# Optimization experiments

Hardware: AMD Instinct MI355X
Metric: run time of the kernel (lower is better)

## Reference

```python
import jax, jax.numpy as jnp
import numpy as np

B, S, D, H = 2, 2048, 2048, 16
NOPE, ROPE, V, C = 128, 64, 128, 512
EPS = 1e-6


def _rope(x, cos, sin):
    # x: [b,s,h,d] with d even; consecutive pairs form complex numbers (torch view_as_complex)
    b, s, h, d = x.shape
    x2 = x.reshape(b, s, h, d // 2, 2)
    xr, xi = x2[..., 0], x2[..., 1]
    c = cos[None, :, None, :]
    sn = sin[None, :, None, :]
    yr = xr * c - xi * sn
    yi = xr * sn + xi * c
    return jnp.stack([yr, yi], axis=-1).reshape(b, s, h, d)


def _rmsnorm(x, w):
    return x * jax.lax.rsqrt(jnp.mean(x * x, axis=-1, keepdims=True) + EPS) * w


def setup_inputs() -> dict:
    key = jax.random.key(0)
    ks = jax.random.split(key, 6)
    x = jax.random.normal(ks[0], (B, S, D), jnp.float32)
    # xavier-ish scaled weights (torch layout: [out, in])
    wq = jax.random.normal(ks[1], (H * (NOPE + ROPE), D), jnp.float32) * (D ** -0.5)
    wkv_a = jax.random.normal(ks[2], (C + ROPE, D), jnp.float32) * (D ** -0.5)
    kv_norm_w = jnp.ones((C,), jnp.float32)
    wkv_b = jax.random.normal(ks[3], (H * (NOPE + V), C), jnp.float32) * (C ** -0.5)
    wo = jax.random.normal(ks[4], (D, H * V), jnp.float32) * ((H * V) ** -0.5)
    # rope freqs (theta=10000), cos/sin of shape [S, ROPE//2]
    inv = 1.0 / (10000.0 ** (np.arange(0, ROPE, 2, dtype=np.float32) / ROPE))
    ang = np.outer(np.arange(S, dtype=np.float32), inv)
    cos = jnp.asarray(np.cos(ang), jnp.float32)
    sin = jnp.asarray(np.sin(ang), jnp.float32)
    # causal additive mask [S, S]
    idx = jnp.arange(S)
    mask = jnp.where(idx[None, :] <= idx[:, None], 0.0, -1e9).astype(jnp.float32)
    return dict(x=x, cos=cos, sin=sin, mask=mask, wq=wq, wkv_a=wkv_a,
                kv_norm_w=kv_norm_w, wkv_b=wkv_b, wo=wo)


def reference(x, cos, sin, mask, wq, wkv_a, kv_norm_w, wkv_b, wo):
    scale = (NOPE + ROPE) ** -0.5
    # Q projection -> [B,S,H,NOPE+ROPE]
    q = (x @ wq.T).reshape(B, S, H, NOPE + ROPE)
    q_nope, q_pe = q[..., :NOPE], q[..., NOPE:]
    q_pe = _rope(q_pe, cos, sin)
    # low-rank KV latent + shared rope key
    kvr = x @ wkv_a.T                      # [B,S,C+ROPE]
    kv, k_pe = kvr[..., :C], kvr[..., C:]
    k_pe = _rope(k_pe[:, :, None, :], cos, sin)[:, :, 0, :]   # [B,S,ROPE]
    # absorb-mode: fold wkv_b's nope part into q
    wb = wkv_b.reshape(H, NOPE + V, C)
    q_abs = jnp.einsum('bshd,hdc->bshc', q_nope, wb[:, :NOPE])
    kvn = _rmsnorm(kv, kv_norm_w)          # latent cache [B,S,C]
    scores = (jnp.einsum('bshc,btc->bsht', q_abs, kvn)
              + jnp.einsum('bshr,btr->bsht', q_pe, k_pe)) * scale
    scores = scores + mask[None, :, None, :]
    p = jax.nn.softmax(scores.astype(jnp.float32), axis=-1).astype(x.dtype)
    o = jnp.einsum('bsht,btc->bshc', p, kvn)
    o = jnp.einsum('bshc,hdc->bshd', o, wb[:, NOPE:])   # un-absorb value proj
    return o.reshape(B, S, H * V) @ wo.T
```

## Files before the change

### kernel.cpp

```cpp
#include <hip/hip_runtime.h>
#include <hip/hip_bf16.h>

#define B_ 2
#define S_ 2048
#define H_ 16

typedef unsigned short ushort_t;
typedef unsigned int uint_t;
typedef __attribute__((ext_vector_type(8))) short bf16x8;
typedef __attribute__((ext_vector_type(4))) float f32x4;

__device__ __forceinline__ ushort_t f2bf(float f) {
    uint_t u = __float_as_uint(f);
    return (ushort_t)((u + 0x7fffu + ((u >> 16) & 1u)) >> 16);
}
__device__ __forceinline__ float bf2f(ushort_t v) {
    return __uint_as_float(((uint_t)v) << 16);
}

__device__ __forceinline__ void gl_lds16(const ushort_t* g, ushort_t* l) {
    __builtin_amdgcn_global_load_lds(
        (const __attribute__((address_space(1))) unsigned int*)(unsigned long long)g,
        (__attribute__((address_space(3))) unsigned int*)(unsigned int)(unsigned long long)l,
        16, 0, 0);
}

__global__ __launch_bounds__(256) void cast_bf16(const float* __restrict__ src,
                                                 ushort_t* __restrict__ dst, int n)
{
    int i = (blockIdx.x * 256 + threadIdx.x) * 4;
    if (i < n) {
        float4 v = *(const float4*)(src + i);
        ushort_t pk[4] = { f2bf(v.x), f2bf(v.y), f2bf(v.z), f2bf(v.w) };
        *(uint2*)(dst + i) = *(const uint2*)pk;
    }
}

__global__ __launch_bounds__(256) void cast2_bf16(const float* __restrict__ src,
                                                  ushort_t* __restrict__ hi,
                                                  ushort_t* __restrict__ lo, int n)
{
    int i = (blockIdx.x * 256 + threadIdx.x) * 4;
    if (i < n) {
        float4 v = *(const float4*)(src + i);
        float vv[4] = { v.x, v.y, v.z, v.w };
        ushort_t ph[4], pl[4];
#pragma unroll
        for (int k = 0; k < 4; k++) {
            ph[k] = f2bf(vv[k]);
            pl[k] = f2bf(vv[k] - bf2f(ph[k]));
        }
        *(uint2*)(hi + i) = *(const uint2*)ph;
        *(uint2*)(lo + i) = *(const uint2*)pl;
    }
}

__global__ __launch_bounds__(256, 2) void gemm_bf16(const ushort_t* __restrict__ A,
                                                    const ushort_t* __restrict__ Bm,
                                                    float* __restrict__ Cf,
                                                    ushort_t* __restrict__ Cb,
                                                    int M, int N, int K,
                                                    int ldc, int Nreal, int mode)
{
    __shared__ __align__(16) ushort_t As[2][8192];
    __shared__ __align__(16) ushort_t Bs[2][8192];
    const int tid = threadIdx.x;
    const int wv = tid >> 6, lane = tid & 63, l16 = lane & 15, quad = lane >> 4;
    const int wm = wv >> 1, wn = wv & 1;
    const int m0 = blockIdx.y * 128, n0 = blockIdx.x * 128;
    const int srow = lane >> 3;
    const int sch  = ((lane & 7) ^ srow) * 8;

    f32x4 acc[16];
#pragma unroll
    for (int i = 0; i < 16; i++) acc[i] = (f32x4)(0.f);

#pragma unroll
    for (int p = 0; p < 4; p++) {
        int g = wv + p*4, row = g*8 + srow;
        int rowb = n0 + row; if (rowb > Nreal - 1) rowb = Nreal - 1;
        gl_lds16(A  + (size_t)(m0 + row) * K + sch, &As[0][g*512]);
        gl_lds16(Bm + (size_t)rowb * K + sch,       &Bs[0][g*512]);
    }
    __syncthreads();

    int cur = 0;
    for (int k0 = 0; k0 < K; k0 += 64) {
        if (k0 + 64 < K) {
#pragma unroll
            for (int p = 0; p < 4; p++) {
                int g = wv + p*4, row = g*8 + srow;
                int rowb = n0 + row; if (rowb > Nreal - 1) rowb = Nreal - 1;
                gl_lds16(A  + (size_t)(m0 + row) * K + k0 + 64 + sch, &As[cur^1][g*512]);
                gl_lds16(Bm + (size_t)rowb * K + k0 + 64 + sch,       &Bs[cur^1][g*512]);
            }
        }
#pragma unroll
        for (int ks = 0; ks < 2; ks++) {
            bf16x8 af[4], bfr[4];
#pragma unroll
            for (int mt = 0; mt < 4; mt++) {
                int row = wm*64 + mt*16 + l16;
                af[mt] = *(const bf16x8*)(&As[cur][row*64 + (((ks*4+quad) ^ (l16&7))*8)]);
            }
#pragma unroll
            for (int nt = 0; nt < 4; nt++) {
                int row = wn*64 + nt*16 + l16;
                bfr[nt] = *(const bf16x8*)(&Bs[cur][row*64 + (((ks*4+quad) ^ (l16&7))*8)]);
            }
#pragma unroll
            for (int mt = 0; mt < 4; mt++)
#pragma unroll
                for (int nt = 0; nt < 4; nt++)
                    acc[mt*4+nt] = __builtin_amdgcn_mfma_f32_16x16x32_bf16(af[mt], bfr[nt], acc[mt*4+nt], 0, 0, 0);
        }
        __syncthreads();
        cur ^= 1;
    }
#pragma unroll
    for (int mt = 0; mt < 4; mt++)
#pragma unroll
        for (int nt = 0; nt < 4; nt++) {
            int cc = n0 + wn*64 + nt*16 + l16;
            if (cc < Nreal) {
#pragma unroll
                for (int r = 0; r < 4; r++) {
                    size_t rr = m0 + wm*64 + mt*16 + quad*4 + r;
                    float v = acc[mt*4+nt][r];
                    if (mode == 1)      Cb[rr*ldc + cc] = f2bf(v);
                    else if (mode == 2) Cf[rr*ldc + cc] += v;
                    else                Cf[rr*ldc + cc] = v;
                }
            }
        }
}

__global__ __launch_bounds__(256, 2) void gemm_kv3(const ushort_t* __restrict__ Ahg,
                                                   const ushort_t* __restrict__ Alg,
                                                   const ushort_t* __restrict__ Bhg,
                                                   const ushort_t* __restrict__ Blg,
                                                   float* __restrict__ Cf)
{
    __shared__ __align__(16) ushort_t Ah[8192];
    __shared__ __align__(16) ushort_t Al[8192];
    __shared__ __align__(16) ushort_t Bh[8192];
    __shared__ __align__(16) ushort_t Bl[8192];
    const int tid = threadIdx.x;
    const int wv = tid >> 6, lane = tid & 63, l16 = lane & 15, quad = lane >> 4;
    const int wm = wv >> 1, wn = wv & 1;
    const int m0 = blockIdx.y * 128, n0 = blockIdx.x * 128;
    const int srow = lane >> 3;
    const int sch  = ((lane & 7) ^ srow) * 8;
    const int K = 2048;

    f32x4 acc[16];
#pragma unroll
    for (int i = 0; i < 16; i++) acc[i] = (f32x4)(0.f);

    for (int k0 = 0; k0 < K; k0 += 64) {
#pragma unroll
        for (int p = 0; p < 4; p++) {
            int g = wv + p*4, row = g*8 + srow;
            int rowb = n0 + row; if (rowb > 575) rowb = 575;
            gl_lds16(Ahg + (size_t)(m0 + row)*K + k0 + sch, Ah + g*512);
            gl_lds16(Alg + (size_t)(m0 + row)*K + k0 + sch, Al + g*512);
            gl_lds16(Bhg + (size_t)rowb*K + k0 + sch,       Bh + g*512);
            gl_lds16(Blg + (size_t)rowb*K + k0 + sch,       Bl + g*512);
        }
        __syncthreads();
#pragma unroll
        for (int ks = 0; ks < 2; ks++) {
            bf16x8 ah[4], al[4], bh[4], bl[4];
#pragma unroll
            for (int mt = 0; mt < 4; mt++) {
                int off = (wm*64 + mt*16 + l16)*64 + (((ks*4+quad) ^ (l16&7))*8);
                ah[mt] = *(const bf16x8*)(Ah + off);
                al[mt] = *(const bf16x8*)(Al + off);
            }
#pragma unroll
            for (int nt = 0; nt < 4; nt++) {
                int off = (wn*64 + nt*16 + l16)*64 + (((ks*4+quad) ^ (l16&7))*8);
                bh[nt] = *(const bf16x8*)(Bh + off);
                bl[nt] = *(const bf16x8*)(Bl + off);
            }
#pragma unroll
            for (int mt = 0; mt < 4; mt++)
#pragma unroll
                for (int nt = 0; nt < 4; nt++) {
                    acc[mt*4+nt] = __builtin_amdgcn_mfma_f32_16x16x32_bf16(ah[mt], bh[nt], acc[mt*4+nt], 0, 0, 0);
                    acc[mt*4+nt] = __builtin_amdgcn_mfma_f32_16x16x32_bf16(al[mt], bh[nt], acc[mt*4+nt], 0, 0, 0);
                    acc[mt*4+nt] = __builtin_amdgcn_mfma_f32_16x16x32_bf16(ah[mt], bl[nt], acc[mt*4+nt], 0, 0, 0);
                }
        }
        __syncthreads();
    }
#pragma unroll
    for (int mt = 0; mt < 4; mt++)
#pragma unroll
        for (int nt = 0; nt < 4; nt++) {
            int cc = n0 + wn*64 + nt*16 + l16;
            if (cc < 576) {
#pragma unroll
                for (int r = 0; r < 4; r++) {
                    size_t rr = m0 + wm*64 + mt*16 + quad*4 + r;
                    Cf[rr*576 + cc] = acc[mt*4+nt][r];
                }
            }
        }
}

__global__ __launch_bounds__(256, 2) void gemm_vp(const ushort_t* __restrict__ kvnb,
                                                  const ushort_t* __restrict__ wbvB,
                                                  ushort_t* __restrict__ vpT)
{
    __shared__ __align__(16) ushort_t As[2][8192];
    __shared__ __align__(16) ushort_t Bs[2][8192];
    const int tid = threadIdx.x;
    const int wv = tid >> 6, lane = tid & 63, l16 = lane & 15, quad = lane >> 4;
    const int wm = wv >> 1, wn = wv & 1;
    const int m0 = blockIdx.x * 128;
    const int h  = blockIdx.y;
    const ushort_t* Bh = wbvB + h*65536;
    const int srow = lane >> 3;
    const int sch  = ((lane & 7) ^ srow) * 8;

    f32x4 acc[16];
#pragma unroll
    for (int i = 0; i < 16; i++) acc[i] = (f32x4)(0.f);

#pragma unroll
    for (int p = 0; p < 4; p++) {
        int g = wv + p*4, row = g*8 + srow;
        gl_lds16(kvnb + (size_t)(m0 + row)*512 + sch, &As[0][g*512]);
        gl_lds16(Bh   + (size_t)row*512 + sch,        &Bs[0][g*512]);
    }
    __syncthreads();

    int cur = 0;
    for (int k0 = 0; k0 < 512; k0 += 64) {
        if (k0 + 64 < 512) {
#pragma unroll
            for (int p = 0; p < 4; p++) {
                int g = wv + p*4, row = g*8 + srow;
                gl_lds16(kvnb + (size_t)(m0 + row)*512 + k0 + 64 + sch, &As[cur^1][g*512]);
                gl_lds16(Bh   + (size_t)row*512 + k0 + 64 + sch,        &Bs[cur^1][g*512]);
            }
        }
#pragma unroll
        for (int ks = 0; ks < 2; ks++) {
            bf16x8 af[4], bfr[4];
#pragma unroll
            for (int mt = 0; mt < 4; mt++) {
                int row = wm*64 + mt*16 + l16;
                af[mt] = *(const bf16x8*)(&As[cur][row*64 + (((ks*4+quad) ^ (l16&7))*8)]);
            }
#pragma unroll
            for (int nt = 0; nt < 4; nt++) {
                int row = wn*64 + nt*16 + l16;
                bfr[nt] = *(const bf16x8*)(&Bs[cur][row*64 + (((ks*4+quad) ^ (l16&7))*8)]);
            }
#pragma unroll
            for (int mt = 0; mt < 4; mt++)
#pragma unroll
                for (int nt = 0; nt < 4; nt++)
                    acc[mt*4+nt] = __builtin_amdgcn_mfma_f32_16x16x32_bf16(af[mt], bfr[nt], acc[mt*4+nt], 0, 0, 0);
        }
        __syncthreads();
        cur ^= 1;
    }
#pragma unroll
    for (int mt = 0; mt < 4; mt++)
#pragma unroll
        for (int nt = 0; nt < 4; nt++) {
            int rr = m0 + wm*64 + mt*16 + quad*4;
            int bb = rr >> 11, t = rr & 2047;
            int cc = wn*64 + nt*16 + l16;
            ushort_t pk[4];
#pragma unroll
            for (int r = 0; r < 4; r++) pk[r] = f2bf(acc[mt*4+nt][r]);
            *(uint2*)(vpT + ((size_t)((bb*16 + h)*128 + cc))*2048 + t) = *(const uint2*)pk;
        }
}

__global__ __launch_bounds__(256) void prep_wb(const float* __restrict__ wkv_b,
                                               ushort_t* __restrict__ wbkT,
                                               ushort_t* __restrict__ wbvB)
{
    int u = blockIdx.x * 256 + threadIdx.x;
    {
        int h = u >> 16, rem = u & 65535, c = rem >> 7, d = rem & 127;
        wbkT[u] = f2bf(wkv_b[h*131072 + d*512 + c]);
    }
    {
        int h = u >> 16, rem = u & 65535;
        wbvB[u] = f2bf(wkv_b[h*131072 + 65536 + rem]);
    }
}

__global__ __launch_bounds__(256) void kv_norm_rope(const float* __restrict__ kvr,
                                                    const float* __restrict__ w,
                                                    const float* __restrict__ cosT,
                                                    const float* __restrict__ sinT,
                                                    ushort_t* __restrict__ kvnb,
                                                    ushort_t* __restrict__ kpeb)
{
    const int bs   = blockIdx.x * 4 + (threadIdx.x >> 6);
    const int lane = threadIdx.x & 63;
    const int s    = bs & (S_ - 1);
    const float* row = kvr + bs * 576;

    float4 v0 = *(const float4*)(row + lane*8);
    float4 v1 = *(const float4*)(row + lane*8 + 4);
    float ss = v0.x*v0.x + v0.y*v0.y + v0.z*v0.z + v0.w*v0.w
             + v1.x*v1.x + v1.y*v1.y + v1.z*v1.z + v1.w*v1.w;
#pragma unroll
    for (int off = 32; off >= 1; off >>= 1) ss += __shfl_xor(ss, off);
    const float rs = rsqrtf(ss * (1.0f/512.0f) + 1e-6f);

    float4 w0 = *(const float4*)(w + lane*8);
    float4 w1 = *(const float4*)(w + lane*8 + 4);
    float o[8];
    o[0] = v0.x*rs*w0.x; o[1] = v0.y*rs*w0.y; o[2] = v0.z*rs*w0.z; o[3] = v0.w*rs*w0.w;
    o[4] = v1.x*rs*w1.x; o[5] = v1.y*rs*w1.y; o[6] = v1.z*rs*w1.z; o[7] = v1.w*rs*w1.w;

    ushort_t pk[8];
#pragma unroll
    for (int p = 0; p < 8; p++) pk[p] = f2bf(o[p]);
    *(uint4*)(kvnb + (size_t)bs*512 + lane*8) = *(const uint4*)pk;

    if (lane < 32) {
        float xr = row[512 + 2*lane], xi = row[512 + 2*lane + 1];
        float c  = cosT[s*32 + lane], sn = sinT[s*32 + lane];
        ushort_t p2[2] = { f2bf(xr*c - xi*sn), f2bf(xr*sn + xi*c) };
        *(uint_t*)(kpeb + (size_t)bs*64 + 2*lane) = *(const uint_t*)p2;
    }
}

__device__ __forceinline__ void stage_F(const ushort_t* kvn_b, const ushort_t* kpe_b,
                                        ushort_t* ldsb, int t0, int buf,
                                        int w, int l16, int q8e)
{
    ushort_t* Fb = ldsb + buf*18432;
#pragma unroll
    for (int ii = 0; ii < 5; ii++) {
        int i = w + ii*8;
        if (i < 36) {
            int g2 = (i >= 18) ? 1 : 0;
            int ks = i - g2*18;
            int row = t0 + g2*16 + l16;
            const ushort_t* src = (ks < 16)
                ? (kvn_b + (size_t)row*512 + ks*32 + q8e)
                : (kpe_b + (size_t)row*64 + (ks-16)*32 + q8e);
            gl_lds16(src, Fb + i*512);
        }
    }
}

__global__ __launch_bounds__(512, 2) void attn_mfma(
    const ushort_t* __restrict__ qb,
    const ushort_t* __restrict__ kvnb,
    const ushort_t* __restrict__ kpeb,
    const ushort_t* __restrict__ vpT,
    const float* __restrict__ cosT,
    const float* __restrict__ sinT,
    const ushort_t* __restrict__ wbkT,
    ushort_t* __restrict__ ovb)
{
    const int flat = blockIdx.x + 16*blockIdx.y + 256*blockIdx.z;
    const int b    = flat & 1;
    const int rem  = flat >> 1;
    const int h    = rem & 15;
    const int q0   = (15 - (rem >> 4)) << 7;

    const int tid  = threadIdx.x;
    const int w    = tid >> 6;
    const int lane = tid & 63;
    const int l16  = lane & 15;
    const int quad = lane >> 4;
    const int tl   = quad * 4;
    const int lb   = lane & 48;
    const int q8e  = quad * 8;
    const float scale = 0.07216878364870323f;

    __shared__ __align__(16) ushort_t lds[40960];

    const ushort_t* kvn_b = kvnb + (size_t)b*S_*512;
    const ushort_t* kpe_b = kpeb + (size_t)b*S_*64;
    const ushort_t* vpT_h = vpT + (size_t)(b*16 + h)*128*2048;

    const int r0    = q0 + w*16;
    const int rglob = r0 + l16;

    stage_F(kvn_b, kpe_b, lds, 0, 0, w, l16, q8e);

    ushort_t* paw = lds + 18432 + w*2176;
    const ushort_t* qrow = qb + (size_t)(b*S_ + rglob)*3072 + h*192;
    bf16x8 qa[4], qf[18];
#pragma unroll
    for (int ks = 0; ks < 4; ks++)
        qa[ks] = *(const bf16x8*)(qrow + ks*32 + q8e);

    const ushort_t* wbk_h = wbkT + h*65536;
#pragma unroll
    for (int qq = 0; qq < 4; qq++) {
        f32x4 ab[8];
#pragma unroll
        for (int n = 0; n < 8; n++) ab[n] = (f32x4)(0.f);
#pragma unroll
        for (int n = 0; n < 8; n++) {
            const ushort_t* wp = wbk_h + (qq*128 + n*16 + l16)*128 + q8e;
#pragma unroll
            for (int ks = 0; ks < 4; ks++) {
                bf16x8 bw = *(const bf16x8*)(wp + ks*32);
                ab[n] = __builtin_amdgcn_mfma_f32_16x16x32_bf16(qa[ks], bw, ab[n], 0, 0, 0);
            }
        }
        asm volatile("" ::: "memory");
#pragma unroll
        for (int n = 0; n < 8; n++)
#pragma unroll
            for (int r = 0; r < 4; r++)
                paw[(tl + r)*136 + n*16 + l16] = f2bf(ab[n][r] * scale);
        asm volatile("" ::: "memory");
#pragma unroll
        for (int ks2 = 0; ks2 < 4; ks2++)
            qf[qq*4 + ks2] = *(const bf16x8*)(paw + l16*136 + ks2*32 + q8e);
        asm volatile("" ::: "memory");
    }

#pragma unroll
    for (int kk = 0; kk < 2; kk++) {
        int off = kk*32 + q8e;
        uint4 pv4 = *(const uint4*)(qrow + 128 + off);
        const ushort_t* pe = (const ushort_t*)&pv4;
        ushort_t pk[8];
#pragma unroll
        for (int u2 = 0; u2 < 4; u2++) {
            float xr = bf2f(pe[2*u2]), xi = bf2f(pe[2*u2+1]);
            int pi = (off >> 1) + u2;
            float c = cosT[rglob*32 + pi], sn = sinT[rglob*32 + pi];
            pk[2*u2]   = f2bf((xr*c  - xi*sn) * scale);
            pk[2*u2+1] = f2bf((xr*sn + xi*c ) * scale);
        }
        qf[16 + kk] = *(const bf16x8*)pk;
    }
    __syncthreads();

    f32x4 o[8];
#pragma unroll
    for (int n = 0; n < 8; n++) o[n] = (f32x4)(0.f);
    float m_s = -1e30f, l_s = 0.f;

    const int bniter = (q0 >> 5) + 4;
    const int wniter = ((r0 + 15) >> 5) + 1;
    ushort_t* V = lds + 36864;
    int cur = 0;

#pragma unroll 1
    for (int it = 0; it < bniter; it++) {
        const int t0 = it * 32;
        if (it + 1 < bniter)
            stage_F(kvn_b, kpe_b, lds, t0 + 32, cur ^ 1, w, l16, q8e);
        {
            const ushort_t* src = vpT_h + (size_t)(w*16 + l16)*2048 + t0 + q8e;
            gl_lds16(src, V + w*512);
        }

        bf16x8 ap;
        if (it < wniter) {
            const ushort_t* Fb = lds + cur*18432;

            f32x4 s0 = (f32x4)(0.f), s1 = (f32x4)(0.f);
#pragma unroll
            for (int ks = 0; ks < 18; ks++) {
                bf16x8 kf0 = *(const bf16x8*)(Fb + ks*512 + lane*8);
                s0 = __builtin_amdgcn_mfma_f32_16x16x32_bf16(kf0, qf[ks], s0, 0, 0, 0);
                bf16x8 kf1 = *(const bf16x8*)(Fb + 9216 + ks*512 + lane*8);
                s1 = __builtin_amdgcn_mfma_f32_16x16x32_bf16(kf1, qf[ks], s1, 0, 0, 0);
            }

            float pv[8];
            float mx = -1e30f;
#pragma unroll
            for (int reg = 0; reg < 4; reg++) {
                pv[reg]   = ((t0 + tl + reg)      <= rglob) ? s0[reg] : -1e30f;
                pv[4+reg] = ((t0 + 16 + tl + reg) <= rglob) ? s1[reg] : -1e30f;
                mx = fmaxf(mx, fmaxf(pv[reg], pv[4+reg]));
            }
            mx = fmaxf(mx, __shfl_xor(mx, 16));
            mx = fmaxf(mx, __shfl_xor(mx, 32));
            if (!__all(mx <= m_s)) {
                float mn = fmaxf(m_s, mx);
                float al = __expf(m_s - mn);
                m_s = mn;
                l_s *= al;
                f32x4 alv;
#pragma unroll
                for (int reg = 0; reg < 4; reg++) alv[reg] = __shfl(al, lb + tl + reg, 64);
#pragma unroll
                for (int n = 0; n < 8; n++) o[n] *= alv;
            }
            float ps = 0.f;
#pragma unroll
            for (int reg = 0; reg < 8; reg++) {
                pv[reg] = (pv[reg] > -1e29f) ? __expf(pv[reg] - m_s) : 0.f;
                ps += pv[reg];
            }
            ps += __shfl_xor(ps, 16);
            ps += __shfl_xor(ps, 32);
            l_s += ps;

            uint_t p00 = (uint_t)f2bf(pv[0]) | ((uint_t)f2bf(pv[1]) << 16);
            uint_t p01 = (uint_t)f2bf(pv[2]) | ((uint_t)f2bf(pv[3]) << 16);
            uint_t p10 = (uint_t)f2bf(pv[4]) | ((uint_t)f2bf(pv[5]) << 16);
            uint_t p11 = (uint_t)f2bf(pv[6]) | ((uint_t)f2bf(pv[7]) << 16);
            int Sa = l16 + ((lane & 16) << 1);
            int Sb = Sa + 16;
            uint_t xa0 = (uint_t)__shfl((int)p00, Sa, 64);
            uint_t xa1 = (uint_t)__shfl((int)p01, Sa, 64);
            uint_t ya0 = (uint_t)__shfl((int)p10, Sa, 64);
            uint_t ya1 = (uint_t)__shfl((int)p11, Sa, 64);
            uint_t xb0 = (uint_t)__shfl((int)p00, Sb, 64);
            uint_t xb1 = (uint_t)__shfl((int)p01, Sb, 64);
            uint_t yb0 = (uint_t)__shfl((int)p10, Sb, 64);
            uint_t yb1 = (uint_t)__shfl((int)p11, Sb, 64);
            bool g1 = quad >= 2;
            uint4 aw;
            aw.x = g1 ? ya0 : xa0;
            aw.y = g1 ? ya1 : xa1;
            aw.z = g1 ? yb0 : xb0;
            aw.w = g1 ? yb1 : xb1;
            ap = *(const bf16x8*)&aw;
        }
        __syncthreads();

        if (it < wniter) {
#pragma unroll
            for (int n = 0; n < 8; n++) {
                bf16x8 bv = *(const bf16x8*)(V + n*512 + lane*8);
                o[n] = __builtin_amdgcn_mfma_f32_16x16x32_bf16(ap, bv, o[n], 0, 0, 0);
            }
        }
        __syncthreads();
        cur ^= 1;
    }

    float linv = 1.f / l_s;
    f32x4 rlv;
#pragma unroll
    for (int reg = 0; reg < 4; reg++) rlv[reg] = __shfl(linv, lb + tl + reg, 64);

    ushort_t* orow = ovb + (size_t)(b*S_ + r0)*2048 + h*128;
#pragma unroll
    for (int n = 0; n < 8; n++)
#pragma unroll
        for (int reg = 0; reg < 4; reg++)
            orow[(size_t)(tl + reg)*2048 + n*16 + l16] = f2bf(o[n][reg] * rlv[reg]);
}

extern "C" void kernel_launch(void* const* d_in, const int* in_sizes, int n_in,
                              void* d_out, int out_size, void* d_ws, size_t ws_size,
                              hipStream_t stream) {
    const float* x     = (const float*)d_in[0];
    const float* cosT  = (const float*)d_in[1];
    const float* sinT  = (const float*)d_in[2];
    const float* wq    = (const float*)d_in[4];
    const float* wkv_a = (const float*)d_in[5];
    const float* kvw   = (const float*)d_in[6];
    const float* wkv_b = (const float*)d_in[7];
    const float* wo    = (const float*)d_in[8];
    float* out = (float*)d_out;

    ushort_t* qb   = (ushort_t*)d_ws;
    ushort_t* xb   = qb   + 12582912;
    ushort_t* wqb  = xb   + 8388608;
    ushort_t* wob  = wqb  + 6291456;
    ushort_t* ovb  = wob  + 4194304;
    ushort_t* kvnb = ovb  + 8388608;
    ushort_t* kpeb = kvnb + 2097152;
    ushort_t* kvnT = kpeb + 262144;
    ushort_t* wbkT = kvnT + 2097152;
    ushort_t* wbvB = wbkT + 1048576;
    float*    kvr  = (float*)(wbvB + 1048576);

    ushort_t* xlo  = ovb;
    ushort_t* wahi = wqb;
    ushort_t* walo = wqb + 1179648;
    ushort_t* vpT  = xb;

    dim3 blk(256);
    cast2_bf16<<<dim3(8192), blk, 0, stream>>>(x, xb, xlo, 8388608);
    cast_bf16<<<dim3(6144), blk, 0, stream>>>(wq, wqb, 6291456);
    cast_bf16<<<dim3(4096), blk, 0, stream>>>(wo, wob, 4194304);
    prep_wb<<<dim3(4096), blk, 0, stream>>>(wkv_b, wbkT, wbvB);
    gemm_bf16<<<dim3(24, 32), blk, 0, stream>>>(xb, wqb, nullptr, qb, 4096, 3072, 2048, 3072, 3072, 1);
    cast2_bf16<<<dim3(1152), blk, 0, stream>>>(wkv_a, wahi, walo, 1179648);
    gemm_kv3<<<dim3(5, 32), blk, 0, stream>>>(xb, xlo, wahi, walo, kvr);
    kv_norm_rope<<<dim3(1024), blk, 0, stream>>>(kvr, kvw, cosT, sinT, kvnb, kpeb);
    gemm_vp<<<dim3(32, 16), blk, 0, stream>>>(kvnb, wbvB, vpT);
    attn_mfma<<<dim3(16, 16, 2), dim3(512), 0, stream>>>(qb, kvnb, kpeb, vpT, cosT, sinT, wbkT, ovb);
    gemm_bf16<<<dim3(16, 32), blk, 0, stream>>>(ovb, wob, out, nullptr, 4096, 2048, 2048, 2048, 2048, 0);
}
```

Baseline: 573.5 us.

## Double-buffer V tile, drop mid-loop barrier, transpose P via LDS, add setprio

V-tile loads now go through the same double-buffered staging as the K/rope tiles. That removes the barrier between the score and PV phases, leaving one sync per iteration. The eight cross-lane shuffles that transposed P into the MFMA A-operand are replaced by a per-wave LDS scratch write and readback. s_setprio hints are placed around the MFMA bursts. LDS use grows, which may affect the 2-blocks-per-CU occupancy target, and the per-wave scratch readback relies only on compiler memory fences within the wave.

```diff
diff --git a/kernel.cpp b/kernel.cpp
--- a/kernel.cpp
+++ b/kernel.cpp
@@ -336,11 +336,12 @@
     }
 }
 
-__device__ __forceinline__ void stage_F(const ushort_t* kvn_b, const ushort_t* kpe_b,
-                                        ushort_t* ldsb, int t0, int buf,
-                                        int w, int l16, int q8e)
+__device__ __forceinline__ void stage_tile(const ushort_t* kvn_b, const ushort_t* kpe_b,
+                                           const ushort_t* vpT_h, ushort_t* ldsb,
+                                           int t0, int buf, int w, int l16, int q8e)
 {
     ushort_t* Fb = ldsb + buf*18432;
+    ushort_t* Vb = ldsb + 36864 + buf*4096;
 #pragma unroll
     for (int ii = 0; ii < 5; ii++) {
         int i = w + ii*8;
@@ -354,6 +355,10 @@
             gl_lds16(src, Fb + i*512);
         }
     }
+    {
+        const ushort_t* src = vpT_h + (size_t)(w*16 + l16)*2048 + t0 + q8e;
+        gl_lds16(src, Vb + w*512);
+    }
 }
 
 __global__ __launch_bounds__(512, 2) void attn_mfma(
@@ -382,7 +387,7 @@
     const int q8e  = quad * 8;
     const float scale = 0.07216878364870323f;
 
-    __shared__ __align__(16) ushort_t lds[40960];
+    __shared__ __align__(16) ushort_t lds[50176];
 
     const ushort_t* kvn_b = kvnb + (size_t)b*S_*512;
     const ushort_t* kpe_b = kpeb + (size_t)b*S_*64;
@@ -391,7 +396,7 @@
     const int r0    = q0 + w*16;
     const int rglob = r0 + l16;
 
-    stage_F(kvn_b, kpe_b, lds, 0, 0, w, l16, q8e);
+    stage_tile(kvn_b, kpe_b, vpT_h, lds, 0, 0, w, l16, q8e);
 
     ushort_t* paw = lds + 18432 + w*2176;
     const ushort_t* qrow = qb + (size_t)(b*S_ + rglob)*3072 + h*192;
@@ -453,23 +458,20 @@
 
     const int bniter = (q0 >> 5) + 4;
     const int wniter = ((r0 + 15) >> 5) + 1;
-    ushort_t* V = lds + 36864;
+    ushort_t* ptw = lds + 45056 + w*640;
     int cur = 0;
 
 #pragma unroll 1
     for (int it = 0; it < bniter; it++) {
-        const int t0 = it * 32;
         if (it + 1 < bniter)
-            stage_F(kvn_b, kpe_b, lds, t0 + 32, cur ^ 1, w, l16, q8e);
-        {
-            const ushort_t* src = vpT_h + (size_t)(w*16 + l16)*2048 + t0 + q8e;
-            gl_lds16(src, V + w*512);
-        }
-
-        bf16x8 ap;
+            stage_tile(kvn_b, kpe_b, vpT_h, lds, (it+1)*32, cur ^ 1, w, l16, q8e);
+
         if (it < wniter) {
+            const int t0 = it * 32;
             const ushort_t* Fb = lds + cur*18432;
-
+            const ushort_t* Vb = lds + 36864 + cur*4096;
+
+            __builtin_amdgcn_s_setprio(1);
             f32x4 s0 = (f32x4)(0.f), s1 = (f32x4)(0.f);
 #pragma unroll
             for (int ks = 0; ks < 18; ks++) {
@@ -478,6 +480,7 @@
                 bf16x8 kf1 = *(const bf16x8*)(Fb + 9216 + ks*512 + lane*8);
                 s1 = __builtin_amdgcn_mfma_f32_16x16x32_bf16(kf1, qf[ks], s1, 0, 0, 0);
             }
+            __builtin_amdgcn_s_setprio(0);
 
             float pv[8];
             float mx = -1e30f;
@@ -510,36 +513,22 @@
             ps += __shfl_xor(ps, 32);
             l_s += ps;
 
-            uint_t p00 = (uint_t)f2bf(pv[0]) | ((uint_t)f2bf(pv[1]) << 16);
-            uint_t p01 = (uint_t)f2bf(pv[2]) | ((uint_t)f2bf(pv[3]) << 16);
-            uint_t p10 = (uint_t)f2bf(pv[4]) | ((uint_t)f2bf(pv[5]) << 16);
-            uint_t p11 = (uint_t)f2bf(pv[6]) | ((uint_t)f2bf(pv[7]) << 16);
-            int Sa = l16 + ((lane & 16) << 1);
-            int Sb = Sa + 16;
-            uint_t xa0 = (uint_t)__shfl((int)p00, Sa, 64);
-            uint_t xa1 = (uint_t)__shfl((int)p01, Sa, 64);
-            uint_t ya0 = (uint_t)__shfl((int)p10, Sa, 64);
-            uint_t ya1 = (uint_t)__shfl((int)p11, Sa, 64);
-            uint_t xb0 = (uint_t)__shfl((int)p00, Sb, 64);
-            uint_t xb1 = (uint_t)__shfl((int)p01, Sb, 64);
-            uint_t yb0 = (uint_t)__shfl((int)p10, Sb, 64);
-            uint_t yb1 = (uint_t)__shfl((int)p11, Sb, 64);
-            bool g1 = quad >= 2;
-            uint4 aw;
-            aw.x = g1 ? ya0 : xa0;
-            aw.y = g1 ? ya1 : xa1;
-            aw.z = g1 ? yb0 : xb0;
-            aw.w = g1 ? yb1 : xb1;
-            ap = *(const bf16x8*)&aw;
-        }
-        __syncthreads();
-
-        if (it < wniter) {
+            ushort_t pk4[8];
+#pragma unroll
+            for (int reg = 0; reg < 8; reg++) pk4[reg] = f2bf(pv[reg]);
+            *(uint2*)(ptw + l16*40 + tl)      = *(const uint2*)(pk4);
+            *(uint2*)(ptw + l16*40 + 16 + tl) = *(const uint2*)(pk4 + 4);
+            asm volatile("" ::: "memory");
+            bf16x8 ap = *(const bf16x8*)(ptw + l16*40 + q8e);
+            asm volatile("" ::: "memory");
+
+            __builtin_amdgcn_s_setprio(1);
 #pragma unroll
             for (int n = 0; n < 8; n++) {
-                bf16x8 bv = *(const bf16x8*)(V + n*512 + lane*8);
+                bf16x8 bv = *(const bf16x8*)(Vb + n*512 + lane*8);
                 o[n] = __builtin_amdgcn_mfma_f32_16x16x32_bf16(ap, bv, o[n], 0, 0, 0);
             }
+            __builtin_amdgcn_s_setprio(0);
         }
         __syncthreads();
         cur ^= 1;
```

New measurement: 533.1 us. -7.0%, faster.
